# Kernel optimization log

Measured on AMD Instinct MI355X. Metric: run time of the kernel, lower is better.

## Reference

```python
import jax, jax.numpy as jnp
import numpy as np

HEADS = 8
EPS = 1e-5


def _attn_axis(x, axis, wq, wkv, wout, bout):
    # x: (B, C, X, Y, Z); self-attention along `axis`, channels at dim 1.
    perm = [0] + [d for d in (2, 3, 4) if d != axis] + [axis, 1]
    xp = jnp.transpose(x, perm)                    # (B, o1, o2, T, C)
    B, o1, o2, T, C = xp.shape
    xf = xp.reshape(B * o1 * o2, T, C)
    q = xf @ wq.T                                  # (Bf, T, C), no bias
    k, v = jnp.split(xf @ wkv.T, 2, axis=-1)
    e = C // HEADS
    sh = lambda t: t.reshape(t.shape[0], T, HEADS, e)
    q, k, v = sh(q), sh(k), sh(v)
    dots = jnp.einsum('bihe,bjhe->bhij', q, k) * (e ** -0.5)
    attn = jax.nn.softmax(dots, axis=-1)
    o = jnp.einsum('bhij,bjhe->bihe', attn, v).reshape(B * o1 * o2, T, C)
    o = (o @ wout.T + bout).reshape(B, o1, o2, T, C)
    inv = tuple(int(i) for i in np.argsort(perm))
    return jnp.transpose(o, inv)


def _ln(x, g, b):
    m = jnp.mean(x, -1, keepdims=True)
    v = jnp.mean((x - m) ** 2, -1, keepdims=True)
    return (x - m) * jax.lax.rsqrt(v + EPS) * g + b


def setup_inputs() -> dict:
    key = jax.random.key(0)
    B, C, X, Y, Z = 2, 128, 48, 48, 48
    ks = iter(jax.random.split(key, 32))
    n = lambda shape, s=0.02: jax.random.normal(next(ks), shape, jnp.float32) * s
    inp = {}
    inp['x'] = jax.random.normal(next(ks), (B, C, X, Y, Z), jnp.float32)
    inp['px'] = jax.random.normal(next(ks), (1, C, X, 1, 1), jnp.float32)
    inp['py'] = jax.random.normal(next(ks), (1, C, 1, Y, 1), jnp.float32)
    inp['pz'] = jax.random.normal(next(ks), (1, C, 1, 1, Z), jnp.float32)
    for i in range(3):
        inp[f'wq{i}'] = n((C, C))
        inp[f'wkv{i}'] = n((2 * C, C))
        inp[f'wout{i}'] = n((C, C))
        inp[f'bout{i}'] = jnp.zeros((C,), jnp.float32)
    inp['ln_g'] = jnp.ones((C,), jnp.float32)
    inp['ln_b'] = jnp.zeros((C,), jnp.float32)
    inp['w1'] = n((C, C)); inp['b1'] = jnp.zeros((C,), jnp.float32)
    inp['w2'] = n((C, C)); inp['b2'] = jnp.zeros((C,), jnp.float32)
    return inp


def reference(x, px, py, pz,
              wq0, wkv0, wout0, bout0,
              wq1, wkv1, wout1, bout1,
              wq2, wkv2, wout2, bout2,
              ln_g, ln_b, w1, b1, w2, b2):
    # source: x += pos_embedding(x); pos_embedding(x) returns x + px + py + pz
    x = x + (x + px + py + pz)
    a = (_attn_axis(x, 2, wq0, wkv0, wout0, bout0)
         + _attn_axis(x, 3, wq1, wkv1, wout1, bout1)
         + _attn_axis(x, 4, wq2, wkv2, wout2, bout2))
    x = a + x                                      # residual (dropout = identity)
    x = jnp.transpose(x, (0, 2, 3, 4, 1))          # channels last
    x = _ln(x, ln_g, ln_b)
    res = x
    h = jax.nn.relu(x @ w1.T + b1)
    h = h @ w2.T + b2
    x = _ln(h + res, ln_g, ln_b)                   # same LayerNorm weights reused
    return jnp.transpose(x, (0, 4, 1, 2, 3))
```

## Files before the change

kernel.cpp:

```cpp
#include <hip/hip_runtime.h>
#include <hip/hip_bf16.h>

typedef __attribute__((ext_vector_type(8))) short short8;
typedef __attribute__((ext_vector_type(4))) short short4v;
typedef __attribute__((ext_vector_type(4))) float floatx4;

#define XSTR 136
#define VSTR 48
#define SSTR 132
#define MSTR 129

static __device__ __forceinline__ short f2b(float f) {
    __hip_bfloat16 h = __float2bfloat16(f);
    return *reinterpret_cast<short*>(&h);
}
static __device__ __forceinline__ float b2f(short s) {
    unsigned int u = ((unsigned int)(unsigned short)s) << 16;
    return __uint_as_float(u);
}

__global__ __launch_bounds__(256) void prep_weights(
    const float* __restrict__ wq0, const float* __restrict__ wkv0,
    const float* __restrict__ wq1, const float* __restrict__ wkv1,
    const float* __restrict__ wq2, const float* __restrict__ wkv2,
    const float* __restrict__ wout0, const float* __restrict__ wout1,
    const float* __restrict__ wout2, const float* __restrict__ w1,
    const float* __restrict__ w2, short* __restrict__ dst)
{
    const int g = blockIdx.x * 256 + threadIdx.x;
    const float* wqs[3]  = { wq0, wq1, wq2 };
    const float* wkvs[3] = { wkv0, wkv1, wkv2 };
    const float* rest[5] = { wout0, wout1, wout2, w1, w2 };
    float val;
    if (g < 147456) {
        const int a = g / 49152, l = g % 49152;
        val = (l < 16384) ? wqs[a][l] : wkvs[a][l - 16384];
    } else {
        const int l = g - 147456;
        val = rest[l >> 14][l & 16383];
    }
    dst[g] = f2b(val);
}

__global__ __launch_bounds__(256) void prep_x2(
    const float* __restrict__ x, const float* __restrict__ px,
    const float* __restrict__ py, const float* __restrict__ pz,
    short* __restrict__ x2b)
{
    __shared__ float tile[128 * 49];
    const int s = blockIdx.x, tid = threadIdx.x;
    const int b = s / 2304, rr = s % 2304, xx = rr / 48, yy = rr % 48;
    for (int f = tid; f < 1536; f += 256) {
        const int c = f / 12, z4 = (f % 12) * 4;
        const floatx4 xv = *(const floatx4*)(x + (long)(b * 128 + c) * 110592 + xx * 2304 + yy * 48 + z4);
        const float pxy = px[c * 48 + xx] + py[c * 48 + yy];
        #pragma unroll
        for (int j = 0; j < 4; ++j)
            tile[c * 49 + z4 + j] = 2.0f * xv[j] + pxy + pz[c * 48 + z4 + j];
    }
    __syncthreads();
    const long tb = (long)b * 110592 + xx * 2304 + yy * 48;
    for (int f = tid; f < 1536; f += 256) {
        const int t = f >> 5, c4 = (f & 31) << 2;
        short4v pk;
        #pragma unroll
        for (int j = 0; j < 4; ++j) pk[j] = f2b(tile[(c4 + j) * 49 + t]);
        *(short4v*)(x2b + (tb + t) * 128 + c4) = pk;
    }
}

template<int AXIS, int ACC>
__global__ __launch_bounds__(512, 4)
void attn_axis(const short* __restrict__ x2b, const short* __restrict__ wcat,
               const short* __restrict__ woutb, const float* __restrict__ bout,
               short* __restrict__ Ab)
{
    __shared__ __align__(16) char SM[76800];
    short* xs  = (short*)SM;
    short* qs  = (short*)(SM + 13056);
    short* ks  = (short*)(SM + 26112);
    short* vs  = (short*)(SM + 39168);
    short* pb  = (short*)(SM + 51456);
    short* ob  = (short*)(SM + 63744);
    float* stg = (float*)(SM + 13056);

    const int tid  = threadIdx.x;
    const int lane = tid & 63;
    const int wave = tid >> 6;
    const int l15  = lane & 15;
    const int quad = lane >> 4;

    const int s = blockIdx.x;
    const int b = s / 2304, rr = s % 2304, u = rr / 48, v = rr % 48;
    long base; int stride;
    if (AXIS == 0) { base = (long)b * 110592 + u * 48   + v; stride = 2304; }
    else           { base = (long)b * 110592 + u * 2304 + v; stride = 48;   }

    short4v apre[3];
    if (ACC) {
        #pragma unroll
        for (int i = 0; i < 3; ++i) {
            const int f = tid + i * 512;
            const int t = f >> 5, c4 = (f & 31) << 2;
            apre[i] = *(const short4v*)(Ab + (base + (long)t * stride) * 128 + c4);
        }
    }
    short8 bcur[4], bnext[4];
    {
        const short* wp = wcat + (wave * 16 + l15) * 128 + quad * 8;
        #pragma unroll
        for (int k = 0; k < 4; ++k) bcur[k] = *(const short8*)(wp + k * 32);
    }

    for (int f = tid; f < 1536; f += 512) {
        const int t = f >> 5, c4 = (f & 31) << 2;
        *(short4v*)(xs + t * XSTR + c4) =
            *(const short4v*)(x2b + (base + (long)t * stride) * 128 + c4);
    }
    __syncthreads();

    short8 af[3][4];
    #pragma unroll
    for (int mt = 0; mt < 3; ++mt)
        #pragma unroll
        for (int k = 0; k < 4; ++k)
            af[mt][k] = *(const short8*)(xs + (mt * 16 + l15) * XSTR + k * 32 + quad * 8);

    const int n0 = wave * 16 + l15;
    {
        const short* wp = wcat + ((wave + 8) * 16 + l15) * 128 + quad * 8;
        #pragma unroll
        for (int k = 0; k < 4; ++k) bnext[k] = *(const short8*)(wp + k * 32);
        floatx4 acc[3] = {{0,0,0,0},{0,0,0,0},{0,0,0,0}};
        #pragma unroll
        for (int mt = 0; mt < 3; ++mt)
            #pragma unroll
            for (int k = 0; k < 4; ++k)
                acc[mt] = __builtin_amdgcn_mfma_f32_16x16x32_bf16(af[mt][k], bcur[k], acc[mt], 0, 0, 0);
        #pragma unroll
        for (int mt = 0; mt < 3; ++mt) {
            const int rbase = mt * 16 + quad * 4;
            #pragma unroll
            for (int g = 0; g < 4; ++g)
                qs[(rbase + g) * XSTR + n0] = f2b(acc[mt][g] * 0.25f);
        }
    }
    {
        const short* wp = wcat + ((wave + 16) * 16 + l15) * 128 + quad * 8;
        #pragma unroll
        for (int k = 0; k < 4; ++k) bcur[k] = *(const short8*)(wp + k * 32);
        floatx4 acc[3] = {{0,0,0,0},{0,0,0,0},{0,0,0,0}};
        #pragma unroll
        for (int mt = 0; mt < 3; ++mt)
            #pragma unroll
            for (int k = 0; k < 4; ++k)
                acc[mt] = __builtin_amdgcn_mfma_f32_16x16x32_bf16(af[mt][k], bnext[k], acc[mt], 0, 0, 0);
        #pragma unroll
        for (int mt = 0; mt < 3; ++mt) {
            const int rbase = mt * 16 + quad * 4;
            #pragma unroll
            for (int g = 0; g < 4; ++g)
                ks[(rbase + g) * XSTR + n0] = f2b(acc[mt][g]);
        }
    }
    {
        floatx4 acc[3] = {{0,0,0,0},{0,0,0,0},{0,0,0,0}};
        #pragma unroll
        for (int mt = 0; mt < 3; ++mt)
            #pragma unroll
            for (int k = 0; k < 4; ++k)
                acc[mt] = __builtin_amdgcn_mfma_f32_16x16x32_bf16(af[mt][k], bcur[k], acc[mt], 0, 0, 0);
        #pragma unroll
        for (int mt = 0; mt < 3; ++mt) {
            short4v pk;
            #pragma unroll
            for (int g = 0; g < 4; ++g) pk[g] = f2b(acc[mt][g]);
            *(short4v*)(vs + n0 * VSTR + mt * 16 + quad * 4) = pk;
        }
    }

    short* pbw = pb + wave * (16 * VSTR);
    const short8 Z8 = {0,0,0,0,0,0,0,0};
    const int hb = wave * 16;
    short8 bk[3], bv0, bv1;
    #pragma unroll
    for (int nt = 0; nt < 3; ++nt) {
        bk[nt] = Z8;
        if (quad < 2) bk[nt] = *(const short8*)(ks + (nt * 16 + l15) * XSTR + hb + quad * 8);
    }
    bv0 = *(const short8*)(vs + (hb + l15) * VSTR + quad * 8);
    bv1 = Z8;
    if (quad < 2) bv1 = *(const short8*)(vs + (hb + l15) * VSTR + 32 + quad * 8);

    #pragma unroll
    for (int mt = 0; mt < 3; ++mt) {
        short8 aq = Z8;
        if (quad < 2) aq = *(const short8*)(qs + (mt * 16 + l15) * XSTR + hb + quad * 8);
        floatx4 sc[3];
        #pragma unroll
        for (int nt = 0; nt < 3; ++nt) {
            floatx4 z = {0,0,0,0};
            sc[nt] = __builtin_amdgcn_mfma_f32_16x16x32_bf16(aq, bk[nt], z, 0, 0, 0);
        }
        #pragma unroll
        for (int g = 0; g < 4; ++g) {
            const float e0 = __expf(sc[0][g]);
            const float e1 = __expf(sc[1][g]);
            const float e2 = __expf(sc[2][g]);
            float ssum = e0 + e1 + e2;
            ssum += __shfl_xor(ssum, 1, 64);
            ssum += __shfl_xor(ssum, 2, 64);
            ssum += __shfl_xor(ssum, 4, 64);
            ssum += __shfl_xor(ssum, 8, 64);
            const float inv = 1.0f / ssum;
            short* prow = pbw + (quad * 4 + g) * VSTR;
            prow[l15]      = f2b(e0 * inv);
            prow[16 + l15] = f2b(e1 * inv);
            prow[32 + l15] = f2b(e2 * inv);
        }
        floatx4 o = {0,0,0,0};
        {
            short8 ap = *(const short8*)(pbw + l15 * VSTR + quad * 8);
            o = __builtin_amdgcn_mfma_f32_16x16x32_bf16(ap, bv0, o, 0, 0, 0);
            short8 ap1 = Z8;
            if (quad < 2) ap1 = *(const short8*)(pbw + l15 * VSTR + 32 + quad * 8);
            o = __builtin_amdgcn_mfma_f32_16x16x32_bf16(ap1, bv1, o, 0, 0, 0);
        }
        #pragma unroll
        for (int g = 0; g < 4; ++g)
            ob[(mt * 16 + quad * 4 + g) * XSTR + hb + l15] = f2b(o[g]);
    }
    __syncthreads();

    #pragma unroll
    for (int mt = 0; mt < 3; ++mt)
        #pragma unroll
        for (int k = 0; k < 4; ++k)
            af[mt][k] = *(const short8*)(ob + (mt * 16 + l15) * XSTR + k * 32 + quad * 8);
    {
        const int n = wave * 16 + l15;
        short8 bf_[4];
        #pragma unroll
        for (int k = 0; k < 4; ++k)
            bf_[k] = *(const short8*)(woutb + n * 128 + k * 32 + quad * 8);
        floatx4 acc[3] = {{0,0,0,0},{0,0,0,0},{0,0,0,0}};
        #pragma unroll
        for (int mt = 0; mt < 3; ++mt)
            #pragma unroll
            for (int k = 0; k < 4; ++k)
                acc[mt] = __builtin_amdgcn_mfma_f32_16x16x32_bf16(af[mt][k], bf_[k], acc[mt], 0, 0, 0);
        const float bo = bout[n];
        #pragma unroll
        for (int mt = 0; mt < 3; ++mt)
            #pragma unroll
            for (int g = 0; g < 4; ++g)
                stg[(mt * 16 + quad * 4 + g) * SSTR + n] = acc[mt][g] + bo;
    }
    __syncthreads();

    #pragma unroll
    for (int i = 0; i < 3; ++i) {
        const int f = tid + i * 512;
        const int t = f >> 5, c4 = (f & 31) << 2;
        const long gi = (base + (long)t * stride) * 128 + c4;
        const floatx4 vv = *(const floatx4*)(stg + t * SSTR + c4);
        short4v out4;
        if (ACC) {
            #pragma unroll
            for (int j = 0; j < 4; ++j) out4[j] = f2b(b2f(apre[i][j]) + vv[j]);
        } else {
            #pragma unroll
            for (int j = 0; j < 4; ++j) out4[j] = f2b(vv[j]);
        }
        *(short4v*)(Ab + gi) = out4;
    }
}

static __device__ __forceinline__ void ln_stats129(const float* xr, float* mean_,
                                                   float* rstd_, int tid)
{
    if (tid < 192) {
        const int r = tid >> 2, p = tid & 3;
        const float* row = xr + r * MSTR + p * 32;
        float s1 = 0.f, s2 = 0.f;
        #pragma unroll
        for (int c0 = 0; c0 < 32; ++c0) {
            const float xv = row[(c0 + p * 8) & 31];
            s1 += xv; s2 += xv * xv;
        }
        s1 += __shfl_xor(s1, 1, 64); s1 += __shfl_xor(s1, 2, 64);
        s2 += __shfl_xor(s2, 1, 64); s2 += __shfl_xor(s2, 2, 64);
        if (p == 0) {
            const float m = s1 * (1.f / 128.f);
            mean_[r] = m;
            rstd_[r] = rsqrtf(s2 * (1.f / 128.f) - m * m + 1e-5f);
        }
    }
}

__global__ __launch_bounds__(512, 4)
void attn2_mlp(const short* __restrict__ x2b, const short* __restrict__ Ab,
               const short* __restrict__ wcat, const short* __restrict__ woutb,
               const float* __restrict__ bout,
               const float* __restrict__ ln_g, const float* __restrict__ ln_b,
               const short* __restrict__ w1b, const float* __restrict__ b1,
               const short* __restrict__ w2b, const float* __restrict__ b2,
               float* __restrict__ out)
{
    __shared__ __align__(16) char SM[79232];
    short* xs   = (short*)SM;
    short* qs   = (short*)(SM + 13056);
    short* ks   = (short*)(SM + 26112);
    short* vs   = (short*)(SM + 39168);
    short* pb   = (short*)(SM + 51456);
    short* ob   = (short*)(SM + 63744);
    float* xr   = (float*)(SM + 13056);
    short* lnb  = (short*)(SM + 39168);
    short* hbuf = (short*)(SM + 63744);
    float* gs   = (float*)(SM + 76800);
    float* bs   = (float*)(SM + 77312);
    float* b1s  = (float*)(SM + 77824);
    float* b2s  = (float*)(SM + 78336);
    float* mean_ = (float*)(SM + 78848);
    float* rstd_ = (float*)(SM + 79040);

    const int tid  = threadIdx.x;
    const int lane = tid & 63;
    const int wave = tid >> 6;
    const int l15  = lane & 15;
    const int quad = lane >> 4;

    const int s = blockIdx.x;
    const int b = s / 2304, rr = s % 2304, xx = rr / 48, yy = rr % 48;
    const long tb = (long)b * 110592 + xx * 2304 + yy * 48;

    short4v apre[3];
    #pragma unroll
    for (int i = 0; i < 3; ++i) {
        const int f = tid + i * 512;
        const int t = f >> 5, c4 = (f & 31) << 2;
        apre[i] = *(const short4v*)(Ab + (tb + t) * 128 + c4);
    }
    short8 bcur[4], bnext[4];
    {
        const short* wp = wcat + (wave * 16 + l15) * 128 + quad * 8;
        #pragma unroll
        for (int k = 0; k < 4; ++k) bcur[k] = *(const short8*)(wp + k * 32);
    }

    if (tid < 128) {
        gs[tid] = ln_g[tid]; bs[tid] = ln_b[tid];
        b1s[tid] = b1[tid];  b2s[tid] = b2[tid];
    }
    short4v xpre[3];
    #pragma unroll
    for (int i = 0; i < 3; ++i) {
        const int f = tid + i * 512;
        const int t = f >> 5, c4 = (f & 31) << 2;
        xpre[i] = *(const short4v*)(x2b + (tb + t) * 128 + c4);
        *(short4v*)(xs + t * XSTR + c4) = xpre[i];
    }
    __syncthreads();

    short8 af[3][4];
    #pragma unroll
    for (int mt = 0; mt < 3; ++mt)
        #pragma unroll
        for (int k = 0; k < 4; ++k)
            af[mt][k] = *(const short8*)(xs + (mt * 16 + l15) * XSTR + k * 32 + quad * 8);

    const int n0 = wave * 16 + l15;
    {
        const short* wp = wcat + ((wave + 8) * 16 + l15) * 128 + quad * 8;
        #pragma unroll
        for (int k = 0; k < 4; ++k) bnext[k] = *(const short8*)(wp + k * 32);
        floatx4 acc[3] = {{0,0,0,0},{0,0,0,0},{0,0,0,0}};
        #pragma unroll
        for (int mt = 0; mt < 3; ++mt)
            #pragma unroll
            for (int k = 0; k < 4; ++k)
                acc[mt] = __builtin_amdgcn_mfma_f32_16x16x32_bf16(af[mt][k], bcur[k], acc[mt], 0, 0, 0);
        #pragma unroll
        for (int mt = 0; mt < 3; ++mt) {
            const int rbase = mt * 16 + quad * 4;
            #pragma unroll
            for (int g = 0; g < 4; ++g)
                qs[(rbase + g) * XSTR + n0] = f2b(acc[mt][g] * 0.25f);
        }
    }
    {
        const short* wp = wcat + ((wave + 16) * 16 + l15) * 128 + quad * 8;
        #pragma unroll
        for (int k = 0; k < 4; ++k) bcur[k] = *(const short8*)(wp + k * 32);
        floatx4 acc[3] = {{0,0,0,0},{0,0,0,0},{0,0,0,0}};
        #pragma unroll
        for (int mt = 0; mt < 3; ++mt)
            #pragma unroll
            for (int k = 0; k < 4; ++k)
                acc[mt] = __builtin_amdgcn_mfma_f32_16x16x32_bf16(af[mt][k], bnext[k], acc[mt], 0, 0, 0);
        #pragma unroll
        for (int mt = 0; mt < 3; ++mt) {
            const int rbase = mt * 16 + quad * 4;
            #pragma unroll
            for (int g = 0; g < 4; ++g)
                ks[(rbase + g) * XSTR + n0] = f2b(acc[mt][g]);
        }
    }
    {
        floatx4 acc[3] = {{0,0,0,0},{0,0,0,0},{0,0,0,0}};
        #pragma unroll
        for (int mt = 0; mt < 3; ++mt)
            #pragma unroll
            for (int k = 0; k < 4; ++k)
                acc[mt] = __builtin_amdgcn_mfma_f32_16x16x32_bf16(af[mt][k], bcur[k], acc[mt], 0, 0, 0);
        #pragma unroll
        for (int mt = 0; mt < 3; ++mt) {
            short4v pk;
            #pragma unroll
            for (int g = 0; g < 4; ++g) pk[g] = f2b(acc[mt][g]);
            *(short4v*)(vs + n0 * VSTR + mt * 16 + quad * 4) = pk;
        }
    }

    short* pbw = pb + wave * (16 * VSTR);
    const short8 Z8 = {0,0,0,0,0,0,0,0};
    const int hb = wave * 16;
    short8 bk[3], bv0, bv1;
    #pragma unroll
    for (int nt = 0; nt < 3; ++nt) {
        bk[nt] = Z8;
        if (quad < 2) bk[nt] = *(const short8*)(ks + (nt * 16 + l15) * XSTR + hb + quad * 8);
    }
    bv0 = *(const short8*)(vs + (hb + l15) * VSTR + quad * 8);
    bv1 = Z8;
    if (quad < 2) bv1 = *(const short8*)(vs + (hb + l15) * VSTR + 32 + quad * 8);

    #pragma unroll
    for (int mt = 0; mt < 3; ++mt) {
        short8 aq = Z8;
        if (quad < 2) aq = *(const short8*)(qs + (mt * 16 + l15) * XSTR + hb + quad * 8);
        floatx4 sc[3];
        #pragma unroll
        for (int nt = 0; nt < 3; ++nt) {
            floatx4 z = {0,0,0,0};
            sc[nt] = __builtin_amdgcn_mfma_f32_16x16x32_bf16(aq, bk[nt], z, 0, 0, 0);
        }
        #pragma unroll
        for (int g = 0; g < 4; ++g) {
            const float e0 = __expf(sc[0][g]);
            const float e1 = __expf(sc[1][g]);
            const float e2 = __expf(sc[2][g]);
            float ssum = e0 + e1 + e2;
            ssum += __shfl_xor(ssum, 1, 64);
            ssum += __shfl_xor(ssum, 2, 64);
            ssum += __shfl_xor(ssum, 4, 64);
            ssum += __shfl_xor(ssum, 8, 64);
            const float inv = 1.0f / ssum;
            short* prow = pbw + (quad * 4 + g) * VSTR;
            prow[l15]      = f2b(e0 * inv);
            prow[16 + l15] = f2b(e1 * inv);
            prow[32 + l15] = f2b(e2 * inv);
        }
        floatx4 o = {0,0,0,0};
        {
            short8 ap = *(const short8*)(pbw + l15 * VSTR + quad * 8);
            o = __builtin_amdgcn_mfma_f32_16x16x32_bf16(ap, bv0, o, 0, 0, 0);
            short8 ap1 = Z8;
            if (quad < 2) ap1 = *(const short8*)(pbw + l15 * VSTR + 32 + quad * 8);
            o = __builtin_amdgcn_mfma_f32_16x16x32_bf16(ap1, bv1, o, 0, 0, 0);
        }
        #pragma unroll
        for (int g = 0; g < 4; ++g)
            ob[(mt * 16 + quad * 4 + g) * XSTR + hb + l15] = f2b(o[g]);
    }
    __syncthreads();

    #pragma unroll
    for (int mt = 0; mt < 3; ++mt)
        #pragma unroll
        for (int k = 0; k < 4; ++k)
            af[mt][k] = *(const short8*)(ob + (mt * 16 + l15) * XSTR + k * 32 + quad * 8);
    {
        const int n = wave * 16 + l15;
        short8 bf_[4];
        #pragma unroll
        for (int k = 0; k < 4; ++k)
            bf_[k] = *(const short8*)(woutb + n * 128 + k * 32 + quad * 8);
        floatx4 acc[3] = {{0,0,0,0},{0,0,0,0},{0,0,0,0}};
        #pragma unroll
        for (int mt = 0; mt < 3; ++mt)
            #pragma unroll
            for (int k = 0; k < 4; ++k)
                acc[mt] = __builtin_amdgcn_mfma_f32_16x16x32_bf16(af[mt][k], bf_[k], acc[mt], 0, 0, 0);
        const float bo = bout[n];
        #pragma unroll
        for (int mt = 0; mt < 3; ++mt)
            #pragma unroll
            for (int g = 0; g < 4; ++g)
                xr[(mt * 16 + quad * 4 + g) * MSTR + n] = acc[mt][g] + bo;
    }
    __syncthreads();

    #pragma unroll
    for (int i = 0; i < 3; ++i) {
        const int f = tid + i * 512;
        const int t = f >> 5, c4 = (f & 31) << 2;
        float s1 = 0.f, s2 = 0.f;
        #pragma unroll
        for (int j = 0; j < 4; ++j) {
            const float vv = xr[t * MSTR + c4 + j] + b2f(apre[i][j]) + b2f(xpre[i][j]);
            xr[t * MSTR + c4 + j] = vv;
            s1 += vv; s2 += vv * vv;
        }
        s1 += __shfl_xor(s1, 1, 64);  s2 += __shfl_xor(s2, 1, 64);
        s1 += __shfl_xor(s1, 2, 64);  s2 += __shfl_xor(s2, 2, 64);
        s1 += __shfl_xor(s1, 4, 64);  s2 += __shfl_xor(s2, 4, 64);
        s1 += __shfl_xor(s1, 8, 64);  s2 += __shfl_xor(s2, 8, 64);
        s1 += __shfl_xor(s1, 16, 64); s2 += __shfl_xor(s2, 16, 64);
        if ((lane & 31) == 0) {
            const float m = s1 * (1.f / 128.f);
            mean_[t] = m;
            rstd_[t] = rsqrtf(s2 * (1.f / 128.f) - m * m + 1e-5f);
        }
    }
    __syncthreads();

    for (int f = tid; f < 6144; f += 512) {
        const int t = f >> 7, c = f & 127;
        lnb[t * XSTR + c] = f2b((xr[t * MSTR + c] - mean_[t]) * rstd_[t] * gs[c] + bs[c]);
    }
    __syncthreads();

    #pragma unroll
    for (int mt = 0; mt < 3; ++mt)
        #pragma unroll
        for (int k = 0; k < 4; ++k)
            af[mt][k] = *(const short8*)(lnb + (mt * 16 + l15) * XSTR + k * 32 + quad * 8);
    {
        const int n = wave * 16 + l15;
        short8 bf_[4];
        #pragma unroll
        for (int k = 0; k < 4; ++k)
            bf_[k] = *(const short8*)(w1b + n * 128 + k * 32 + quad * 8);
        floatx4 acc[3] = {{0,0,0,0},{0,0,0,0},{0,0,0,0}};
        #pragma unroll
        for (int mt = 0; mt < 3; ++mt)
            #pragma unroll
            for (int k = 0; k < 4; ++k)
                acc[mt] = __builtin_amdgcn_mfma_f32_16x16x32_bf16(af[mt][k], bf_[k], acc[mt], 0, 0, 0);
        const float bb = b1s[n];
        #pragma unroll
        for (int mt = 0; mt < 3; ++mt)
            #pragma unroll
            for (int g = 0; g < 4; ++g)
                hbuf[(mt * 16 + quad * 4 + g) * XSTR + n] = f2b(fmaxf(acc[mt][g] + bb, 0.f));
    }
    __syncthreads();

    #pragma unroll
    for (int mt = 0; mt < 3; ++mt)
        #pragma unroll
        for (int k = 0; k < 4; ++k)
            af[mt][k] = *(const short8*)(hbuf + (mt * 16 + l15) * XSTR + k * 32 + quad * 8);
    {
        const int n = wave * 16 + l15;
        short8 bf_[4];
        #pragma unroll
        for (int k = 0; k < 4; ++k)
            bf_[k] = *(const short8*)(w2b + n * 128 + k * 32 + quad * 8);
        floatx4 acc[3] = {{0,0,0,0},{0,0,0,0},{0,0,0,0}};
        #pragma unroll
        for (int mt = 0; mt < 3; ++mt)
            #pragma unroll
            for (int k = 0; k < 4; ++k)
                acc[mt] = __builtin_amdgcn_mfma_f32_16x16x32_bf16(af[mt][k], bf_[k], acc[mt], 0, 0, 0);
        const float bb = b2s[n];
        #pragma unroll
        for (int mt = 0; mt < 3; ++mt)
            #pragma unroll
            for (int g = 0; g < 4; ++g) {
                const int t = mt * 16 + quad * 4 + g;
                const float ln1 = (xr[t * MSTR + n] - mean_[t]) * rstd_[t] * gs[n] + bs[n];
                xr[t * MSTR + n] = acc[mt][g] + bb + ln1;
            }
    }
    __syncthreads();
    ln_stats129(xr, mean_, rstd_, tid);
    __syncthreads();

    for (int f = tid; f < 1536; f += 512) {
        const int c = f / 12, z4 = (f % 12) * 4;
        floatx4 o4;
        #pragma unroll
        for (int j = 0; j < 4; ++j)
            o4[j] = (xr[(z4 + j) * MSTR + c] - mean_[z4 + j]) * rstd_[z4 + j] * gs[c] + bs[c];
        *(floatx4*)(out + (long)(b * 128 + c) * 110592 + xx * 2304 + yy * 48 + z4) = o4;
    }
}

extern "C" void kernel_launch(void* const* d_in, const int* in_sizes, int n_in,
                              void* d_out, int out_size, void* d_ws, size_t ws_size,
                              hipStream_t stream)
{
    const float* x    = (const float*)d_in[0];
    const float* px   = (const float*)d_in[1];
    const float* py   = (const float*)d_in[2];
    const float* pz   = (const float*)d_in[3];
    const float* wq[3]   = { (const float*)d_in[4],  (const float*)d_in[8],  (const float*)d_in[12] };
    const float* wkv[3]  = { (const float*)d_in[5],  (const float*)d_in[9],  (const float*)d_in[13] };
    const float* wout[3] = { (const float*)d_in[6],  (const float*)d_in[10], (const float*)d_in[14] };
    const float* bout[3] = { (const float*)d_in[7],  (const float*)d_in[11], (const float*)d_in[15] };
    const float* ln_g = (const float*)d_in[16];
    const float* ln_b = (const float*)d_in[17];
    const float* w1   = (const float*)d_in[18];
    const float* b1   = (const float*)d_in[19];
    const float* w2   = (const float*)d_in[20];
    const float* b2   = (const float*)d_in[21];

    short* Ab  = (short*)d_ws;
    short* wb  = (short*)((char*)d_ws + 56623104);
    short* x2b = (short*)((char*)d_ws + 57081856);

    prep_weights<<<896, 256, 0, stream>>>(wq[0], wkv[0], wq[1], wkv[1], wq[2], wkv[2],
                                          wout[0], wout[1], wout[2], w1, w2, wb);
    prep_x2<<<4608, 256, 0, stream>>>(x, px, py, pz, x2b);

    attn_axis<0, 0><<<4608, 512, 0, stream>>>(x2b, wb,         wb + 147456, bout[0], Ab);
    attn_axis<1, 1><<<4608, 512, 0, stream>>>(x2b, wb + 49152, wb + 163840, bout[1], Ab);

    attn2_mlp<<<4608, 512, 0, stream>>>(x2b, Ab, wb + 98304, wb + 180224, bout[2],
                                        ln_g, ln_b, wb + 196608, b1, wb + 212992, b2,
                                        (float*)d_out);
}
```

Measured before the change: 601.6 us.

## Transpose MFMA operand order so outputs store as packed vectors to LDS

Swaps the A/B operands of the projection, attention and MLP MFMAs so each lane's accumulator holds consecutive output channels. Results can then go to shared memory as short4/float4 vector stores instead of scalar strided stores. Q/K are kept in per-wave head-local transposed buffers, and the softmax reduction now runs over lanes 16/32 apart. Shared-memory strides change (VSTR 56, MSTR 132) to keep vector alignment and limit bank conflicts, at the cost of slightly more LDS per block.

```diff
diff --git a/kernel.cpp b/kernel.cpp
--- a/kernel.cpp
+++ b/kernel.cpp
@@ -6,9 +6,10 @@
 typedef __attribute__((ext_vector_type(4))) float floatx4;
 
 #define XSTR 136
-#define VSTR 48
+#define HSTR 16
+#define VSTR 56
 #define SSTR 132
-#define MSTR 129
+#define MSTR 132
 
 static __device__ __forceinline__ short f2b(float f) {
     __hip_bfloat16 h = __float2bfloat16(f);
@@ -75,13 +76,13 @@
                const short* __restrict__ woutb, const float* __restrict__ bout,
                short* __restrict__ Ab)
 {
-    __shared__ __align__(16) char SM[76800];
+    __shared__ __align__(16) char SM[79360];
     short* xs  = (short*)SM;
-    short* qs  = (short*)(SM + 13056);
-    short* ks  = (short*)(SM + 26112);
-    short* vs  = (short*)(SM + 39168);
-    short* pb  = (short*)(SM + 51456);
-    short* ob  = (short*)(SM + 63744);
+    short* qsT = (short*)(SM + 13056);
+    short* ksT = (short*)(SM + 25344);
+    short* vs  = (short*)(SM + 37632);
+    short* pb  = (short*)(SM + 51968);
+    short* obT = (short*)(SM + 66304);
     float* stg = (float*)(SM + 13056);
 
     const int tid  = threadIdx.x;
@@ -105,11 +106,11 @@
             apre[i] = *(const short4v*)(Ab + (base + (long)t * stride) * 128 + c4);
         }
     }
-    short8 bcur[4], bnext[4];
+    short8 wq_[4], wk_[4], wv_[4];
     {
         const short* wp = wcat + (wave * 16 + l15) * 128 + quad * 8;
         #pragma unroll
-        for (int k = 0; k < 4; ++k) bcur[k] = *(const short8*)(wp + k * 32);
+        for (int k = 0; k < 4; ++k) wq_[k] = *(const short8*)(wp + k * 32);
     }
 
     for (int f = tid; f < 1536; f += 512) {
@@ -121,140 +122,139 @@
 
     short8 af[3][4];
     #pragma unroll
-    for (int mt = 0; mt < 3; ++mt)
+    for (int ct = 0; ct < 3; ++ct)
         #pragma unroll
         for (int k = 0; k < 4; ++k)
-            af[mt][k] = *(const short8*)(xs + (mt * 16 + l15) * XSTR + k * 32 + quad * 8);
-
-    const int n0 = wave * 16 + l15;
+            af[ct][k] = *(const short8*)(xs + (ct * 16 + l15) * XSTR + k * 32 + quad * 8);
+
+    short* qw  = qsT + wave * (48 * HSTR);
+    short* kw  = ksT + wave * (48 * HSTR);
+    const int hb = wave * 16;
+
     {
         const short* wp = wcat + ((wave + 8) * 16 + l15) * 128 + quad * 8;
         #pragma unroll
-        for (int k = 0; k < 4; ++k) bnext[k] = *(const short8*)(wp + k * 32);
+        for (int k = 0; k < 4; ++k) wk_[k] = *(const short8*)(wp + k * 32);
+        floatx4 acc[3] = {{0,0,0,0},{0,0,0,0},{0,0,0,0}};
+        #pragma unroll
+        for (int ct = 0; ct < 3; ++ct)
+            #pragma unroll
+            for (int k = 0; k < 4; ++k)
+                acc[ct] = __builtin_amdgcn_mfma_f32_16x16x32_bf16(wq_[k], af[ct][k], acc[ct], 0, 0, 0);
+        #pragma unroll
+        for (int ct = 0; ct < 3; ++ct) {
+            short4v pk;
+            #pragma unroll
+            for (int g = 0; g < 4; ++g) pk[g] = f2b(acc[ct][g] * 0.25f);
+            *(short4v*)(qw + (ct * 16 + l15) * HSTR + quad * 4) = pk;
+        }
+    }
+    {
+        const short* wp = wcat + ((wave + 16) * 16 + l15) * 128 + quad * 8;
+        #pragma unroll
+        for (int k = 0; k < 4; ++k) wv_[k] = *(const short8*)(wp + k * 32);
+        floatx4 acc[3] = {{0,0,0,0},{0,0,0,0},{0,0,0,0}};
+        #pragma unroll
+        for (int ct = 0; ct < 3; ++ct)
+            #pragma unroll
+            for (int k = 0; k < 4; ++k)
+                acc[ct] = __builtin_amdgcn_mfma_f32_16x16x32_bf16(wk_[k], af[ct][k], acc[ct], 0, 0, 0);
+        #pragma unroll
+        for (int ct = 0; ct < 3; ++ct) {
+            short4v pk;
+            #pragma unroll
+            for (int g = 0; g < 4; ++g) pk[g] = f2b(acc[ct][g]);
+            *(short4v*)(kw + (ct * 16 + l15) * HSTR + quad * 4) = pk;
+        }
+    }
+    {
         floatx4 acc[3] = {{0,0,0,0},{0,0,0,0},{0,0,0,0}};
         #pragma unroll
         for (int mt = 0; mt < 3; ++mt)
             #pragma unroll
             for (int k = 0; k < 4; ++k)
-                acc[mt] = __builtin_amdgcn_mfma_f32_16x16x32_bf16(af[mt][k], bcur[k], acc[mt], 0, 0, 0);
+                acc[mt] = __builtin_amdgcn_mfma_f32_16x16x32_bf16(af[mt][k], wv_[k], acc[mt], 0, 0, 0);
         #pragma unroll
         for (int mt = 0; mt < 3; ++mt) {
-            const int rbase = mt * 16 + quad * 4;
-            #pragma unroll
-            for (int g = 0; g < 4; ++g)
-                qs[(rbase + g) * XSTR + n0] = f2b(acc[mt][g] * 0.25f);
-        }
-    }
-    {
-        const short* wp = wcat + ((wave + 16) * 16 + l15) * 128 + quad * 8;
-        #pragma unroll
-        for (int k = 0; k < 4; ++k) bcur[k] = *(const short8*)(wp + k * 32);
-        floatx4 acc[3] = {{0,0,0,0},{0,0,0,0},{0,0,0,0}};
-        #pragma unroll
-        for (int mt = 0; mt < 3; ++mt)
-            #pragma unroll
-            for (int k = 0; k < 4; ++k)
-                acc[mt] = __builtin_amdgcn_mfma_f32_16x16x32_bf16(af[mt][k], bnext[k], acc[mt], 0, 0, 0);
-        #pragma unroll
-        for (int mt = 0; mt < 3; ++mt) {
-            const int rbase = mt * 16 + quad * 4;
-            #pragma unroll
-            for (int g = 0; g < 4; ++g)
-                ks[(rbase + g) * XSTR + n0] = f2b(acc[mt][g]);
-        }
-    }
-    {
-        floatx4 acc[3] = {{0,0,0,0},{0,0,0,0},{0,0,0,0}};
-        #pragma unroll
-        for (int mt = 0; mt < 3; ++mt)
-            #pragma unroll
-            for (int k = 0; k < 4; ++k)
-                acc[mt] = __builtin_amdgcn_mfma_f32_16x16x32_bf16(af[mt][k], bcur[k], acc[mt], 0, 0, 0);
-        #pragma unroll
-        for (int mt = 0; mt < 3; ++mt) {
             short4v pk;
             #pragma unroll
             for (int g = 0; g < 4; ++g) pk[g] = f2b(acc[mt][g]);
-            *(short4v*)(vs + n0 * VSTR + mt * 16 + quad * 4) = pk;
+            *(short4v*)(vs + (hb + l15) * VSTR + mt * 16 + quad * 4) = pk;
         }
     }
 
     short* pbw = pb + wave * (16 * VSTR);
     const short8 Z8 = {0,0,0,0,0,0,0,0};
-    const int hb = wave * 16;
-    short8 bk[3], bv0, bv1;
-    #pragma unroll
-    for (int nt = 0; nt < 3; ++nt) {
-        bk[nt] = Z8;
-        if (quad < 2) bk[nt] = *(const short8*)(ks + (nt * 16 + l15) * XSTR + hb + quad * 8);
-    }
-    bv0 = *(const short8*)(vs + (hb + l15) * VSTR + quad * 8);
-    bv1 = Z8;
-    if (quad < 2) bv1 = *(const short8*)(vs + (hb + l15) * VSTR + 32 + quad * 8);
-
-    #pragma unroll
-    for (int mt = 0; mt < 3; ++mt) {
-        short8 aq = Z8;
-        if (quad < 2) aq = *(const short8*)(qs + (mt * 16 + l15) * XSTR + hb + quad * 8);
+    short8 akf[3], aqf[3];
+    #pragma unroll
+    for (int t = 0; t < 3; ++t) {
+        akf[t] = (quad < 2) ? *(const short8*)(kw + (t * 16 + l15) * HSTR + quad * 8) : Z8;
+        aqf[t] = (quad < 2) ? *(const short8*)(qw + (t * 16 + l15) * HSTR + quad * 8) : Z8;
+    }
+    short8 av0 = *(const short8*)(vs + (hb + l15) * VSTR + quad * 8);
+    short8 av1 = (quad < 2) ? *(const short8*)(vs + (hb + l15) * VSTR + 32 + quad * 8) : Z8;
+
+    #pragma unroll
+    for (int it = 0; it < 3; ++it) {
         floatx4 sc[3];
         #pragma unroll
-        for (int nt = 0; nt < 3; ++nt) {
+        for (int jt = 0; jt < 3; ++jt) {
             floatx4 z = {0,0,0,0};
-            sc[nt] = __builtin_amdgcn_mfma_f32_16x16x32_bf16(aq, bk[nt], z, 0, 0, 0);
-        }
-        #pragma unroll
-        for (int g = 0; g < 4; ++g) {
-            const float e0 = __expf(sc[0][g]);
-            const float e1 = __expf(sc[1][g]);
-            const float e2 = __expf(sc[2][g]);
-            float ssum = e0 + e1 + e2;
-            ssum += __shfl_xor(ssum, 1, 64);
-            ssum += __shfl_xor(ssum, 2, 64);
-            ssum += __shfl_xor(ssum, 4, 64);
-            ssum += __shfl_xor(ssum, 8, 64);
-            const float inv = 1.0f / ssum;
-            short* prow = pbw + (quad * 4 + g) * VSTR;
-            prow[l15]      = f2b(e0 * inv);
-            prow[16 + l15] = f2b(e1 * inv);
-            prow[32 + l15] = f2b(e2 * inv);
-        }
+            sc[jt] = __builtin_amdgcn_mfma_f32_16x16x32_bf16(akf[jt], aqf[it], z, 0, 0, 0);
+        }
+        float e[3][4]; float ssum = 0.f;
+        #pragma unroll
+        for (int jt = 0; jt < 3; ++jt)
+            #pragma unroll
+            for (int g = 0; g < 4; ++g) { e[jt][g] = __expf(sc[jt][g]); ssum += e[jt][g]; }
+        ssum += __shfl_xor(ssum, 16, 64);
+        ssum += __shfl_xor(ssum, 32, 64);
+        const float inv = 1.0f / ssum;
+        #pragma unroll
+        for (int jt = 0; jt < 3; ++jt) {
+            short4v pk;
+            #pragma unroll
+            for (int g = 0; g < 4; ++g) pk[g] = f2b(e[jt][g] * inv);
+            *(short4v*)(pbw + l15 * VSTR + jt * 16 + quad * 4) = pk;
+        }
+        short8 ap  = *(const short8*)(pbw + l15 * VSTR + quad * 8);
+        short8 ap1 = (quad < 2) ? *(const short8*)(pbw + l15 * VSTR + 32 + quad * 8) : Z8;
         floatx4 o = {0,0,0,0};
-        {
-            short8 ap = *(const short8*)(pbw + l15 * VSTR + quad * 8);
-            o = __builtin_amdgcn_mfma_f32_16x16x32_bf16(ap, bv0, o, 0, 0, 0);
-            short8 ap1 = Z8;
-            if (quad < 2) ap1 = *(const short8*)(pbw + l15 * VSTR + 32 + quad * 8);
-            o = __builtin_amdgcn_mfma_f32_16x16x32_bf16(ap1, bv1, o, 0, 0, 0);
-        }
-        #pragma unroll
-        for (int g = 0; g < 4; ++g)
-            ob[(mt * 16 + quad * 4 + g) * XSTR + hb + l15] = f2b(o[g]);
-    }
-    __syncthreads();
-
-    #pragma unroll
-    for (int mt = 0; mt < 3; ++mt)
+        o = __builtin_amdgcn_mfma_f32_16x16x32_bf16(av0, ap,  o, 0, 0, 0);
+        o = __builtin_amdgcn_mfma_f32_16x16x32_bf16(av1, ap1, o, 0, 0, 0);
+        short4v ok;
+        #pragma unroll
+        for (int g = 0; g < 4; ++g) ok[g] = f2b(o[g]);
+        *(short4v*)(obT + (it * 16 + l15) * XSTR + hb + quad * 4) = ok;
+    }
+    __syncthreads();
+
+    short8 afo[3][4];
+    #pragma unroll
+    for (int ct = 0; ct < 3; ++ct)
         #pragma unroll
         for (int k = 0; k < 4; ++k)
-            af[mt][k] = *(const short8*)(ob + (mt * 16 + l15) * XSTR + k * 32 + quad * 8);
-    {
-        const int n = wave * 16 + l15;
-        short8 bf_[4];
+            afo[ct][k] = *(const short8*)(obT + (ct * 16 + l15) * XSTR + k * 32 + quad * 8);
+    {
+        const int nf = wave * 16;
+        short8 wo_[4];
         #pragma unroll
         for (int k = 0; k < 4; ++k)
-            bf_[k] = *(const short8*)(woutb + n * 128 + k * 32 + quad * 8);
-        floatx4 acc[3] = {{0,0,0,0},{0,0,0,0},{0,0,0,0}};
-        #pragma unroll
-        for (int mt = 0; mt < 3; ++mt)
-            #pragma unroll
-            for (int k = 0; k < 4; ++k)
-                acc[mt] = __builtin_amdgcn_mfma_f32_16x16x32_bf16(af[mt][k], bf_[k], acc[mt], 0, 0, 0);
-        const float bo = bout[n];
-        #pragma unroll
-        for (int mt = 0; mt < 3; ++mt)
-            #pragma unroll
-            for (int g = 0; g < 4; ++g)
-                stg[(mt * 16 + quad * 4 + g) * SSTR + n] = acc[mt][g] + bo;
+            wo_[k] = *(const short8*)(woutb + (nf + l15) * 128 + k * 32 + quad * 8);
+        floatx4 acc[3] = {{0,0,0,0},{0,0,0,0},{0,0,0,0}};
+        #pragma unroll
+        for (int ct = 0; ct < 3; ++ct)
+            #pragma unroll
+            for (int k = 0; k < 4; ++k)
+                acc[ct] = __builtin_amdgcn_mfma_f32_16x16x32_bf16(wo_[k], afo[ct][k], acc[ct], 0, 0, 0);
+        const floatx4 bo4 = *(const floatx4*)(bout + nf + quad * 4);
+        #pragma unroll
+        for (int ct = 0; ct < 3; ++ct) {
+            floatx4 ox;
+            #pragma unroll
+            for (int g = 0; g < 4; ++g) ox[g] = acc[ct][g] + bo4[g];
+            *(floatx4*)(stg + (ct * 16 + l15) * SSTR + nf + quad * 4) = ox;
+        }
     }
     __syncthreads();
 
@@ -276,7 +276,7 @@
     }
 }
 
-static __device__ __forceinline__ void ln_stats129(const float* xr, float* mean_,
+static __device__ __forceinline__ void ln_stats132(const float* xr, float* mean_,
                                                    float* rstd_, int tid)
 {
     if (tid < 192) {
@@ -307,22 +307,22 @@
                const short* __restrict__ w2b, const float* __restrict__ b2,
                float* __restrict__ out)
 {
-    __shared__ __align__(16) char SM[79232];
+    __shared__ __align__(16) char SM[81792];
     short* xs   = (short*)SM;
-    short* qs   = (short*)(SM + 13056);
-    short* ks   = (short*)(SM + 26112);
-    short* vs   = (short*)(SM + 39168);
-    short* pb   = (short*)(SM + 51456);
-    short* ob   = (short*)(SM + 63744);
+    short* qsT  = (short*)(SM + 13056);
+    short* ksT  = (short*)(SM + 25344);
+    short* vs   = (short*)(SM + 37632);
+    short* pb   = (short*)(SM + 51968);
+    short* obT  = (short*)(SM + 66304);
     float* xr   = (float*)(SM + 13056);
-    short* lnb  = (short*)(SM + 39168);
-    short* hbuf = (short*)(SM + 63744);
-    float* gs   = (float*)(SM + 76800);
-    float* bs   = (float*)(SM + 77312);
-    float* b1s  = (float*)(SM + 77824);
-    float* b2s  = (float*)(SM + 78336);
-    float* mean_ = (float*)(SM + 78848);
-    float* rstd_ = (float*)(SM + 79040);
+    short* lnb  = (short*)(SM + 38400);
+    short* hbuf = (short*)(SM + 66304);
+    float* gs   = (float*)(SM + 79360);
+    float* bs   = (float*)(SM + 79872);
+    float* b1s  = (float*)(SM + 80384);
+    float* b2s  = (float*)(SM + 80896);
+    float* mean_ = (float*)(SM + 81408);
+    float* rstd_ = (float*)(SM + 81600);
 
     const int tid  = threadIdx.x;
     const int lane = tid & 63;
@@ -341,11 +341,11 @@
         const int t = f >> 5, c4 = (f & 31) << 2;
         apre[i] = *(const short4v*)(Ab + (tb + t) * 128 + c4);
     }
-    short8 bcur[4], bnext[4];
+    short8 wq_[4], wk_[4], wv_[4];
     {
         const short* wp = wcat + (wave * 16 + l15) * 128 + quad * 8;
         #pragma unroll
-        for (int k = 0; k < 4; ++k) bcur[k] = *(const short8*)(wp + k * 32);
+        for (int k = 0; k < 4; ++k) wq_[k] = *(const short8*)(wp + k * 32);
     }
 
     if (tid < 128) {
@@ -364,140 +364,139 @@
 
     short8 af[3][4];
     #pragma unroll
-    for (int mt = 0; mt < 3; ++mt)
+    for (int ct = 0; ct < 3; ++ct)
         #pragma unroll
         for (int k = 0; k < 4; ++k)
-            af[mt][k] = *(const short8*)(xs + (mt * 16 + l15) * XSTR + k * 32 + quad * 8);
-
-    const int n0 = wave * 16 + l15;
+            af[ct][k] = *(const short8*)(xs + (ct * 16 + l15) * XSTR + k * 32 + quad * 8);
+
+    short* qw  = qsT + wave * (48 * HSTR);
+    short* kw  = ksT + wave * (48 * HSTR);
+    const int hb = wave * 16;
+
     {
         const short* wp = wcat + ((wave + 8) * 16 + l15) * 128 + quad * 8;
         #pragma unroll
-        for (int k = 0; k < 4; ++k) bnext[k] = *(const short8*)(wp + k * 32);
+        for (int k = 0; k < 4; ++k) wk_[k] = *(const short8*)(wp + k * 32);
+        floatx4 acc[3] = {{0,0,0,0},{0,0,0,0},{0,0,0,0}};
+        #pragma unroll
+        for (int ct = 0; ct < 3; ++ct)
+            #pragma unroll
+            for (int k = 0; k < 4; ++k)
+                acc[ct] = __builtin_amdgcn_mfma_f32_16x16x32_bf16(wq_[k], af[ct][k], acc[ct], 0, 0, 0);
+        #pragma unroll
+        for (int ct = 0; ct < 3; ++ct) {
+            short4v pk;
+            #pragma unroll
+            for (int g = 0; g < 4; ++g) pk[g] = f2b(acc[ct][g] * 0.25f);
+            *(short4v*)(qw + (ct * 16 + l15) * HSTR + quad * 4) = pk;
+        }
+    }
+    {
+        const short* wp = wcat + ((wave + 16) * 16 + l15) * 128 + quad * 8;
+        #pragma unroll
+        for (int k = 0; k < 4; ++k) wv_[k] = *(const short8*)(wp + k * 32);
+        floatx4 acc[3] = {{0,0,0,0},{0,0,0,0},{0,0,0,0}};
+        #pragma unroll
+        for (int ct = 0; ct < 3; ++ct)
+            #pragma unroll
+            for (int k = 0; k < 4; ++k)
+                acc[ct] = __builtin_amdgcn_mfma_f32_16x16x32_bf16(wk_[k], af[ct][k], acc[ct], 0, 0, 0);
+        #pragma unroll
+        for (int ct = 0; ct < 3; ++ct) {
+            short4v pk;
+            #pragma unroll
+            for (int g = 0; g < 4; ++g) pk[g] = f2b(acc[ct][g]);
+            *(short4v*)(kw + (ct * 16 + l15) * HSTR + quad * 4) = pk;
+        }
+    }
+    {
         floatx4 acc[3] = {{0,0,0,0},{0,0,0,0},{0,0,0,0}};
         #pragma unroll
         for (int mt = 0; mt < 3; ++mt)
             #pragma unroll
             for (int k = 0; k < 4; ++k)
-                acc[mt] = __builtin_amdgcn_mfma_f32_16x16x32_bf16(af[mt][k], bcur[k], acc[mt], 0, 0, 0);
+                acc[mt] = __builtin_amdgcn_mfma_f32_16x16x32_bf16(af[mt][k], wv_[k], acc[mt], 0, 0, 0);
         #pragma unroll
         for (int mt = 0; mt < 3; ++mt) {
-            const int rbase = mt * 16 + quad * 4;
-            #pragma unroll
-            for (int g = 0; g < 4; ++g)
-                qs[(rbase + g) * XSTR + n0] = f2b(acc[mt][g] * 0.25f);
-        }
-    }
-    {
-        const short* wp = wcat + ((wave + 16) * 16 + l15) * 128 + quad * 8;
-        #pragma unroll
-        for (int k = 0; k < 4; ++k) bcur[k] = *(const short8*)(wp + k * 32);
-        floatx4 acc[3] = {{0,0,0,0},{0,0,0,0},{0,0,0,0}};
-        #pragma unroll
-        for (int mt = 0; mt < 3; ++mt)
-            #pragma unroll
-            for (int k = 0; k < 4; ++k)
-                acc[mt] = __builtin_amdgcn_mfma_f32_16x16x32_bf16(af[mt][k], bnext[k], acc[mt], 0, 0, 0);
-        #pragma unroll
-        for (int mt = 0; mt < 3; ++mt) {
-            const int rbase = mt * 16 + quad * 4;
-            #pragma unroll
-            for (int g = 0; g < 4; ++g)
-                ks[(rbase + g) * XSTR + n0] = f2b(acc[mt][g]);
-        }
-    }
-    {
-        floatx4 acc[3] = {{0,0,0,0},{0,0,0,0},{0,0,0,0}};
-        #pragma unroll
-        for (int mt = 0; mt < 3; ++mt)
-            #pragma unroll
-            for (int k = 0; k < 4; ++k)
-                acc[mt] = __builtin_amdgcn_mfma_f32_16x16x32_bf16(af[mt][k], bcur[k], acc[mt], 0, 0, 0);
-        #pragma unroll
-        for (int mt = 0; mt < 3; ++mt) {
             short4v pk;
             #pragma unroll
             for (int g = 0; g < 4; ++g) pk[g] = f2b(acc[mt][g]);
-            *(short4v*)(vs + n0 * VSTR + mt * 16 + quad * 4) = pk;
+            *(short4v*)(vs + (hb + l15) * VSTR + mt * 16 + quad * 4) = pk;
         }
     }
 
     short* pbw = pb + wave * (16 * VSTR);
     const short8 Z8 = {0,0,0,0,0,0,0,0};
-    const int hb = wave * 16;
-    short8 bk[3], bv0, bv1;
-    #pragma unroll
-    for (int nt = 0; nt < 3; ++nt) {
-        bk[nt] = Z8;
-        if (quad < 2) bk[nt] = *(const short8*)(ks + (nt * 16 + l15) * XSTR + hb + quad * 8);
-    }
-    bv0 = *(const short8*)(vs + (hb + l15) * VSTR + quad * 8);
-    bv1 = Z8;
-    if (quad < 2) bv1 = *(const short8*)(vs + (hb + l15) * VSTR + 32 + quad * 8);
-
-    #pragma unroll
-    for (int mt = 0; mt < 3; ++mt) {
-        short8 aq = Z8;
-        if (quad < 2) aq = *(const short8*)(qs + (mt * 16 + l15) * XSTR + hb + quad * 8);
+    short8 akf[3], aqf[3];
+    #pragma unroll
+    for (int t = 0; t < 3; ++t) {
+        akf[t] = (quad < 2) ? *(const short8*)(kw + (t * 16 + l15) * HSTR + quad * 8) : Z8;
+        aqf[t] = (quad < 2) ? *(const short8*)(qw + (t * 16 + l15) * HSTR + quad * 8) : Z8;
+    }
+    short8 av0 = *(const short8*)(vs + (hb + l15) * VSTR + quad * 8);
+    short8 av1 = (quad < 2) ? *(const short8*)(vs + (hb + l15) * VSTR + 32 + quad * 8) : Z8;
+
+    #pragma unroll
+    for (int it = 0; it < 3; ++it) {
         floatx4 sc[3];
         #pragma unroll
-        for (int nt = 0; nt < 3; ++nt) {
+        for (int jt = 0; jt < 3; ++jt) {
             floatx4 z = {0,0,0,0};
-            sc[nt] = __builtin_amdgcn_mfma_f32_16x16x32_bf16(aq, bk[nt], z, 0, 0, 0);
-        }
-        #pragma unroll
-        for (int g = 0; g < 4; ++g) {
-            const float e0 = __expf(sc[0][g]);
-            const float e1 = __expf(sc[1][g]);
-            const float e2 = __expf(sc[2][g]);
-            float ssum = e0 + e1 + e2;
-            ssum += __shfl_xor(ssum, 1, 64);
-            ssum += __shfl_xor(ssum, 2, 64);
-            ssum += __shfl_xor(ssum, 4, 64);
-            ssum += __shfl_xor(ssum, 8, 64);
-            const float inv = 1.0f / ssum;
-            short* prow = pbw + (quad * 4 + g) * VSTR;
-            prow[l15]      = f2b(e0 * inv);
-            prow[16 + l15] = f2b(e1 * inv);
-            prow[32 + l15] = f2b(e2 * inv);
-        }
+            sc[jt] = __builtin_amdgcn_mfma_f32_16x16x32_bf16(akf[jt], aqf[it], z, 0, 0, 0);
+        }
+        float e[3][4]; float ssum = 0.f;
+        #pragma unroll
+        for (int jt = 0; jt < 3; ++jt)
+            #pragma unroll
+            for (int g = 0; g < 4; ++g) { e[jt][g] = __expf(sc[jt][g]); ssum += e[jt][g]; }
+        ssum += __shfl_xor(ssum, 16, 64);
+        ssum += __shfl_xor(ssum, 32, 64);
+        const float inv = 1.0f / ssum;
+        #pragma unroll
+        for (int jt = 0; jt < 3; ++jt) {
+            short4v pk;
+            #pragma unroll
+            for (int g = 0; g < 4; ++g) pk[g] = f2b(e[jt][g] * inv);
+            *(short4v*)(pbw + l15 * VSTR + jt * 16 + quad * 4) = pk;
+        }
+        short8 ap  = *(const short8*)(pbw + l15 * VSTR + quad * 8);
+        short8 ap1 = (quad < 2) ? *(const short8*)(pbw + l15 * VSTR + 32 + quad * 8) : Z8;
         floatx4 o = {0,0,0,0};
-        {
-            short8 ap = *(const short8*)(pbw + l15 * VSTR + quad * 8);
-            o = __builtin_amdgcn_mfma_f32_16x16x32_bf16(ap, bv0, o, 0, 0, 0);
-            short8 ap1 = Z8;
-            if (quad < 2) ap1 = *(const short8*)(pbw + l15 * VSTR + 32 + quad * 8);
-            o = __builtin_amdgcn_mfma_f32_16x16x32_bf16(ap1, bv1, o, 0, 0, 0);
-        }
-        #pragma unroll
-        for (int g = 0; g < 4; ++g)
-            ob[(mt * 16 + quad * 4 + g) * XSTR + hb + l15] = f2b(o[g]);
-    }
-    __syncthreads();
-
-    #pragma unroll
-    for (int mt = 0; mt < 3; ++mt)
+        o = __builtin_amdgcn_mfma_f32_16x16x32_bf16(av0, ap,  o, 0, 0, 0);
+        o = __builtin_amdgcn_mfma_f32_16x16x32_bf16(av1, ap1, o, 0, 0, 0);
+        short4v ok;
+        #pragma unroll
+        for (int g = 0; g < 4; ++g) ok[g] = f2b(o[g]);
+        *(short4v*)(obT + (it * 16 + l15) * XSTR + hb + quad * 4) = ok;
+    }
+    __syncthreads();
+
+    const int nf = wave * 16;
+    {
+        short8 afo[3][4];
+        #pragma unroll
+        for (int ct = 0; ct < 3; ++ct)
+            #pragma unroll
+            for (int k = 0; k < 4; ++k)
+                afo[ct][k] = *(const short8*)(obT + (ct * 16 + l15) * XSTR + k * 32 + quad * 8);
+        short8 wo_[4];
         #pragma unroll
         for (int k = 0; k < 4; ++k)
-            af[mt][k] = *(const short8*)(ob + (mt * 16 + l15) * XSTR + k * 32 + quad * 8);
-    {
-        const int n = wave * 16 + l15;
-        short8 bf_[4];
-        #pragma unroll
-        for (int k = 0; k < 4; ++k)
-            bf_[k] = *(const short8*)(woutb + n * 128 + k * 32 + quad * 8);
-        floatx4 acc[3] = {{0,0,0,0},{0,0,0,0},{0,0,0,0}};
-        #pragma unroll
-        for (int mt = 0; mt < 3; ++mt)
-            #pragma unroll
-            for (int k = 0; k < 4; ++k)
-                acc[mt] = __builtin_amdgcn_mfma_f32_16x16x32_bf16(af[mt][k], bf_[k], acc[mt], 0, 0, 0);
-        const float bo = bout[n];
-        #pragma unroll
-        for (int mt = 0; mt < 3; ++mt)
-            #pragma unroll
-            for (int g = 0; g < 4; ++g)
-                xr[(mt * 16 + quad * 4 + g) * MSTR + n] = acc[mt][g] + bo;
+            wo_[k] = *(const short8*)(woutb + (nf + l15) * 128 + k * 32 + quad * 8);
+        floatx4 acc[3] = {{0,0,0,0},{0,0,0,0},{0,0,0,0}};
+        #pragma unroll
+        for (int ct = 0; ct < 3; ++ct)
+            #pragma unroll
+            for (int k = 0; k < 4; ++k)
+                acc[ct] = __builtin_amdgcn_mfma_f32_16x16x32_bf16(wo_[k], afo[ct][k], acc[ct], 0, 0, 0);
+        const floatx4 bo4 = *(const floatx4*)(bout + nf + quad * 4);
+        #pragma unroll
+        for (int ct = 0; ct < 3; ++ct) {
+            floatx4 ox;
+            #pragma unroll
+            for (int g = 0; g < 4; ++g) ox[g] = acc[ct][g] + bo4[g];
+            *(floatx4*)(xr + (ct * 16 + l15) * MSTR + nf + quad * 4) = ox;
+        }
     }
     __syncthreads();
 
@@ -505,13 +504,14 @@
     for (int i = 0; i < 3; ++i) {
         const int f = tid + i * 512;
         const int t = f >> 5, c4 = (f & 31) << 2;
+        floatx4 xv = *(const floatx4*)(xr + t * MSTR + c4);
         float s1 = 0.f, s2 = 0.f;
         #pragma unroll
         for (int j = 0; j < 4; ++j) {
-            const float vv = xr[t * MSTR + c4 + j] + b2f(apre[i][j]) + b2f(xpre[i][j]);
-            xr[t * MSTR + c4 + j] = vv;
-            s1 += vv; s2 += vv * vv;
-        }
+            xv[j] += b2f(apre[i][j]) + b2f(xpre[i][j]);
+            s1 += xv[j]; s2 += xv[j] * xv[j];
+        }
+        *(floatx4*)(xr + t * MSTR + c4) = xv;
         s1 += __shfl_xor(s1, 1, 64);  s2 += __shfl_xor(s2, 1, 64);
         s1 += __shfl_xor(s1, 2, 64);  s2 += __shfl_xor(s2, 2, 64);
         s1 += __shfl_xor(s1, 4, 64);  s2 += __shfl_xor(s2, 4, 64);
@@ -531,61 +531,70 @@
     }
     __syncthreads();
 
-    #pragma unroll
-    for (int mt = 0; mt < 3; ++mt)
+    {
+        short8 afl[3][4];
+        #pragma unroll
+        for (int ct = 0; ct < 3; ++ct)
+            #pragma unroll
+            for (int k = 0; k < 4; ++k)
+                afl[ct][k] = *(const short8*)(lnb + (ct * 16 + l15) * XSTR + k * 32 + quad * 8);
+        short8 w1_[4];
         #pragma unroll
         for (int k = 0; k < 4; ++k)
-            af[mt][k] = *(const short8*)(lnb + (mt * 16 + l15) * XSTR + k * 32 + quad * 8);
-    {
-        const int n = wave * 16 + l15;
-        short8 bf_[4];
+            w1_[k] = *(const short8*)(w1b + (nf + l15) * 128 + k * 32 + quad * 8);
+        floatx4 acc[3] = {{0,0,0,0},{0,0,0,0},{0,0,0,0}};
+        #pragma unroll
+        for (int ct = 0; ct < 3; ++ct)
+            #pragma unroll
+            for (int k = 0; k < 4; ++k)
+                acc[ct] = __builtin_amdgcn_mfma_f32_16x16x32_bf16(w1_[k], afl[ct][k], acc[ct], 0, 0, 0);
+        const floatx4 bb4 = *(const floatx4*)(b1s + nf + quad * 4);
+        #pragma unroll
+        for (int ct = 0; ct < 3; ++ct) {
+            short4v hk;
+            #pragma unroll
+            for (int g = 0; g < 4; ++g) hk[g] = f2b(fmaxf(acc[ct][g] + bb4[g], 0.f));
+            *(short4v*)(hbuf + (ct * 16 + l15) * XSTR + nf + quad * 4) = hk;
+        }
+    }
+    __syncthreads();
+
+    {
+        short8 afh[3][4];
+        #pragma unroll
+        for (int ct = 0; ct < 3; ++ct)
+            #pragma unroll
+            for (int k = 0; k < 4; ++k)
+                afh[ct][k] = *(const short8*)(hbuf + (ct * 16 + l15) * XSTR + k * 32 + quad * 8);
+        short8 w2_[4];
         #pragma unroll
         for (int k = 0; k < 4; ++k)
-            bf_[k] = *(const short8*)(w1b + n * 128 + k * 32 + quad * 8);
-        floatx4 acc[3] = {{0,0,0,0},{0,0,0,0},{0,0,0,0}};
-        #pragma unroll
-        for (int mt = 0; mt < 3; ++mt)
-            #pragma unroll
-            for (int k = 0; k < 4; ++k)
-                acc[mt] = __builtin_amdgcn_mfma_f32_16x16x32_bf16(af[mt][k], bf_[k], acc[mt], 0, 0, 0);
-        const float bb = b1s[n];
-        #pragma unroll
-        for (int mt = 0; mt < 3; ++mt)
-            #pragma unroll
-            for (int g = 0; g < 4; ++g)
-                hbuf[(mt * 16 + quad * 4 + g) * XSTR + n] = f2b(fmaxf(acc[mt][g] + bb, 0.f));
-    }
-    __syncthreads();
-
-    #pragma unroll
-    for (int mt = 0; mt < 3; ++mt)
-        #pragma unroll
-        for (int k = 0; k < 4; ++k)
-            af[mt][k] = *(const short8*)(hbuf + (mt * 16 + l15) * XSTR + k * 32 + quad * 8);
-    {
-        const int n = wave * 16 + l15;
-        short8 bf_[4];
-        #pragma unroll
-        for (int k = 0; k < 4; ++k)
-            bf_[k] = *(const short8*)(w2b + n * 128 + k * 32 + quad * 8);
-        floatx4 acc[3] = {{0,0,0,0},{0,0,0,0},{0,0,0,0}};
-        #pragma unroll
-        for (int mt = 0; mt < 3; ++mt)
-            #pragma unroll
-            for (int k = 0; k < 4; ++k)
-                acc[mt] = __builtin_amdgcn_mfma_f32_16x16x32_bf16(af[mt][k], bf_[k], acc[mt], 0, 0, 0);
-        const float bb = b2s[n];
-        #pragma unroll
-        for (int mt = 0; mt < 3; ++mt)
+            w2_[k] = *(const short8*)(w2b + (nf + l15) * 128 + k * 32 + quad * 8);
+        floatx4 acc[3] = {{0,0,0,0},{0,0,0,0},{0,0,0,0}};
+        #pragma unroll
+        for (int ct = 0; ct < 3; ++ct)
+            #pragma unroll
+            for (int k = 0; k < 4; ++k)
+                acc[ct] = __builtin_amdgcn_mfma_f32_16x16x32_bf16(w2_[k], afh[ct][k], acc[ct], 0, 0, 0);
+        const floatx4 bb4 = *(const floatx4*)(b2s + nf + quad * 4);
+        const floatx4 g4  = *(const floatx4*)(gs + nf + quad * 4);
+        const floatx4 be4 = *(const floatx4*)(bs + nf + quad * 4);
+        #pragma unroll
+        for (int ct = 0; ct < 3; ++ct) {
+            const int t = ct * 16 + l15;
+            const float mn = mean_[t], rs = rstd_[t];
+            floatx4 xv = *(const floatx4*)(xr + t * MSTR + nf + quad * 4);
+            floatx4 nx;
             #pragma unroll
             for (int g = 0; g < 4; ++g) {
-                const int t = mt * 16 + quad * 4 + g;
-                const float ln1 = (xr[t * MSTR + n] - mean_[t]) * rstd_[t] * gs[n] + bs[n];
-                xr[t * MSTR + n] = acc[mt][g] + bb + ln1;
+                const float ln1 = (xv[g] - mn) * rs * g4[g] + be4[g];
+                nx[g] = acc[ct][g] + bb4[g] + ln1;
             }
-    }
-    __syncthreads();
-    ln_stats129(xr, mean_, rstd_, tid);
+            *(floatx4*)(xr + t * MSTR + nf + quad * 4) = nx;
+        }
+    }
+    __syncthreads();
+    ln_stats132(xr, mean_, rstd_, tid);
     __syncthreads();
 
     for (int f = tid; f < 1536; f += 512) {
```

Result: faster. 575.0 us (-4.4%).
